# Optimization experiments

Measured on AMD Instinct MI355X. Metric: run time of the kernel, lower is better.

Reference implementation:

```python
import jax, jax.numpy as jnp
import numpy as np

B, S, D, H = 8, 1024, 1024, 16
DH = D // H


def setup_inputs() -> dict:
    key = jax.random.key(0)
    ks = jax.random.split(key, 7)
    scale = 1.0 / np.sqrt(DH)
    return {
        "sequences": jax.random.normal(ks[0], (B, S, D), dtype=jnp.float32),
        "Wq": jax.random.uniform(ks[1], (H, DH, DH), jnp.float32, -scale, scale),
        "bq": jax.random.uniform(ks[2], (H, DH), jnp.float32, -scale, scale),
        "Wk": jax.random.uniform(ks[3], (H, DH, DH), jnp.float32, -scale, scale),
        "bk": jax.random.uniform(ks[4], (H, DH), jnp.float32, -scale, scale),
        "Wv": jax.random.uniform(ks[5], (H, DH, DH), jnp.float32, -scale, scale),
        "bv": jax.random.uniform(ks[6], (H, DH), jnp.float32, -scale, scale),
    }


def reference(sequences, Wq, bq, Wk, bk, Wv, bv):
    # split channels into heads: [B,S,H,DH]
    x = sequences.reshape(B, S, H, DH)
    # per-head linear maps (torch Linear: y = x @ W.T + b)
    q = jnp.einsum("bshd,hed->bshe", x, Wq) + bq  # [B,S,H,DH]
    k = jnp.einsum("bshd,hed->bshe", x, Wk) + bk
    v = jnp.einsum("bshd,hed->bshe", x, Wv) + bv
    scores = jnp.einsum("bshd,bthd->bhst", q, k) / jnp.sqrt(jnp.asarray(DH, x.dtype))
    attn = jax.nn.softmax(scores, axis=-1)  # [B,H,S,S]
    out = jnp.einsum("bhst,bthd->bshd", attn, v)  # [B,S,H,DH]
    return out.reshape(B, S, D)
```

## Files before the change

### kernel.cpp

```cpp
#include <hip/hip_runtime.h>
#include <hip/hip_bf16.h>


constexpr int NB = 8, NS = 1024, ND = 1024, NH = 16, NDH = 64;

typedef __bf16 bf16x8 __attribute__((ext_vector_type(8)));
typedef float f32x4 __attribute__((ext_vector_type(4)));

__device__ __forceinline__ f32x4 mfma16(bf16x8 a, bf16x8 b, f32x4 c) {
  return __builtin_amdgcn_mfma_f32_16x16x32_bf16(a, b, c, 0, 0, 0);
}

__device__ __forceinline__ bf16x8 cvt2bf8(float4 lo, float4 hi) {
  bf16x8 r;
  r[0] = (__bf16)lo.x; r[1] = (__bf16)lo.y; r[2] = (__bf16)lo.z; r[3] = (__bf16)lo.w;
  r[4] = (__bf16)hi.x; r[5] = (__bf16)hi.y; r[6] = (__bf16)hi.z; r[7] = (__bf16)hi.w;
  return r;
}

__device__ __forceinline__ void gload16(const __hip_bfloat16* g, __hip_bfloat16* l) {
  __builtin_amdgcn_global_load_lds(
      (const __attribute__((address_space(1))) void*)g,
      (__attribute__((address_space(3))) void*)l, 16, 0, 0);
}

__global__ __launch_bounds__(256) void qkv_proj_kernel(
    const float* __restrict__ x,
    const float* __restrict__ Wq, const float* __restrict__ bq,
    const float* __restrict__ Wk, const float* __restrict__ bk,
    const float* __restrict__ Wv, const float* __restrict__ bv,
    __hip_bfloat16* __restrict__ Qo, __hip_bfloat16* __restrict__ Ko,
    __hip_bfloat16* __restrict__ Vt) {
  __shared__ __align__(16) __hip_bfloat16 Wlds[3][NDH][72];
  const int tid = threadIdx.x;
  const int wave = tid >> 6, lane = tid & 63;
  const int m = lane & 15, quad = lane >> 4;
  const int h = blockIdx.x & (NH - 1);
  const int sblk = blockIdx.x >> 4;

  const float* Ws[3] = {Wq + h * 4096, Wk + h * 4096, Wv + h * 4096};
#pragma unroll
  for (int mt = 0; mt < 3; mt++) {
#pragma unroll
    for (int p = 0; p < 4; p++) {
      int idx = (p * 256 + tid) * 4;
      float4 v = *(const float4*)(Ws[mt] + idx);
      __align__(8) __hip_bfloat16 t4[4] = {
          __float2bfloat16(v.x), __float2bfloat16(v.y),
          __float2bfloat16(v.z), __float2bfloat16(v.w)};
      *(uint2*)&Wlds[mt][idx >> 6][idx & 63] = *(const uint2*)t4;
    }
  }
  __syncthreads();

  float bq4[4][4], bk4[4][4], bvv[4];
#pragma unroll
  for (int nt = 0; nt < 4; nt++) {
    float4 a = *(const float4*)(bq + h * 64 + nt * 16 + quad * 4);
    float4 c = *(const float4*)(bk + h * 64 + nt * 16 + quad * 4);
    bq4[nt][0] = a.x; bq4[nt][1] = a.y; bq4[nt][2] = a.z; bq4[nt][3] = a.w;
    bk4[nt][0] = c.x; bk4[nt][1] = c.y; bk4[nt][2] = c.z; bk4[nt][3] = c.w;
    bvv[nt] = bv[h * 64 + nt * 16 + m];
  }

  const int rowbase = sblk * 256 + wave * 64;
  bf16x8 Xf[4][2];
#pragma unroll
  for (int st = 0; st < 4; st++) {
    const float* xp = x + (size_t)(rowbase + st * 16 + m) * ND + h * NDH + quad * 8;
#pragma unroll
    for (int c = 0; c < 2; c++) {
      float4 lo = *(const float4*)(xp + c * 32);
      float4 hi = *(const float4*)(xp + c * 32 + 4);
      Xf[st][c] = cvt2bf8(lo, hi);
    }
  }

  const int b = rowbase >> 10;
  const int s0 = rowbase & 1023;
  const float qscale = 0.18033688011112042f;

#pragma unroll
  for (int mt = 0; mt < 3; mt++) {
#pragma unroll
    for (int nt = 0; nt < 4; nt++) {
      bf16x8 w0 = *(const bf16x8*)&Wlds[mt][nt * 16 + m][quad * 8];
      bf16x8 w1 = *(const bf16x8*)&Wlds[mt][nt * 16 + m][32 + quad * 8];
#pragma unroll
      for (int st = 0; st < 4; st++) {
        f32x4 acc = {0.f, 0.f, 0.f, 0.f};
        if (mt < 2) {
          acc = mfma16(w0, Xf[st][0], acc);
          acc = mfma16(w1, Xf[st][1], acc);
          const int srow = s0 + st * 16 + m;
          __align__(8) __hip_bfloat16 t4[4];
          if (mt == 0) {
#pragma unroll
            for (int r = 0; r < 4; r++)
              t4[r] = __float2bfloat16((acc[r] + bq4[nt][r]) * qscale);
            *(uint2*)(Qo + ((size_t)(b * NH + h) * NS + srow) * NDH +
                      nt * 16 + quad * 4) = *(const uint2*)t4;
          } else {
#pragma unroll
            for (int r = 0; r < 4; r++)
              t4[r] = __float2bfloat16(acc[r] + bk4[nt][r]);
            *(uint2*)(Ko + ((size_t)(b * NH + h) * NS + srow) * NDH +
                      nt * 16 + quad * 4) = *(const uint2*)t4;
          }
        } else {
          acc = mfma16(Xf[st][0], w0, acc);
          acc = mfma16(Xf[st][1], w1, acc);
          __align__(8) __hip_bfloat16 t4[4];
#pragma unroll
          for (int r = 0; r < 4; r++) t4[r] = __float2bfloat16(acc[r] + bvv[nt]);
          *(uint2*)(Vt + ((size_t)(b * NH + h) * NDH + nt * 16 + m) * NS + s0 +
                    st * 16 + quad * 4) = *(const uint2*)t4;
        }
      }
    }
  }
}

__global__ __launch_bounds__(256, 3) void attn_kernel(
    const __hip_bfloat16* __restrict__ Q,
    const __hip_bfloat16* __restrict__ K,
    const __hip_bfloat16* __restrict__ Vt,
    float* __restrict__ out) {
  __shared__ __align__(16) __hip_bfloat16 Kt[2][64][64];
  __shared__ __align__(16) __hip_bfloat16 Vl[2][64][64];
  __shared__ __align__(16) __hip_bfloat16 Pt[4][2][16][64];

  const int tid = threadIdx.x;
  const int wave = tid >> 6, lane = tid & 63;
  const int m = lane & 15, quad = lane >> 4;

  const int xcd = blockIdx.x & 7;
  const int j = blockIdx.x >> 3;
  const int bh = xcd * 16 + (j & 15);
  const int qblk = j >> 4;
  const int qbase = qblk * 128 + wave * 32;

  const __hip_bfloat16* Qp = Q + (size_t)bh * NS * NDH;
  const __hip_bfloat16* Kp = K + (size_t)bh * NS * NDH;
  const __hip_bfloat16* Vp = Vt + (size_t)bh * NDH * NS;

  bf16x8 Bq[2][2];
#pragma unroll
  for (int g = 0; g < 2; g++)
#pragma unroll
    for (int c = 0; c < 2; c++)
      Bq[g][c] = *(const bf16x8*)(Qp + (size_t)(qbase + g * 16 + m) * NDH +
                                  c * 32 + quad * 8);

  f32x4 accO[2][4];
  f32x4 lsum[2];
#pragma unroll
  for (int g = 0; g < 2; g++) {
    lsum[g] = (f32x4){0.f, 0.f, 0.f, 0.f};
#pragma unroll
    for (int nt = 0; nt < 4; nt++) accO[g][nt] = (f32x4){0.f, 0.f, 0.f, 0.f};
  }
  bf16x8 ones;
#pragma unroll
  for (int i = 0; i < 8; i++) ones[i] = (__bf16)1.0f;

  const int r8 = lane >> 3;
  const int cs = (lane & 7) ^ r8;
  const int pc = quad ^ (m & 7);

#define STAGE(buf, tb)                                                        \
  {                                                                           \
    _Pragma("unroll") for (int p = 0; p < 2; p++) {                           \
      const int row = wave * 16 + p * 8;                                      \
      gload16(Kp + (size_t)((tb) * 64 + row + r8) * NDH + cs * 8,             \
              &Kt[buf][row][0]);                                              \
      gload16(Vp + (size_t)(row + r8) * NS + (tb) * 64 + cs * 8,              \
              &Vl[buf][row][0]);                                              \
    }                                                                         \
  }

  STAGE(0, 0);

  for (int tb = 0; tb < NS / 64; tb++) {
    const int cur = tb & 1;
    __syncthreads();
    if (tb + 1 < NS / 64) STAGE(cur ^ 1, tb + 1);

    f32x4 sc[2][4];
#pragma unroll
    for (int nt = 0; nt < 4; nt++) {
      bf16x8 k0 = *(const bf16x8*)&Kt[cur][nt * 16 + m][pc * 8];
      bf16x8 k1 = *(const bf16x8*)&Kt[cur][nt * 16 + m][(pc ^ 4) * 8];
#pragma unroll
      for (int g = 0; g < 2; g++) {
        f32x4 a = {0.f, 0.f, 0.f, 0.f};
        a = mfma16(k0, Bq[g][0], a);
        a = mfma16(k1, Bq[g][1], a);
        sc[g][nt] = a;
      }
    }
#pragma unroll
    for (int g = 0; g < 2; g++) {
#pragma unroll
      for (int nt = 0; nt < 4; nt++) {
        __align__(8) __hip_bfloat16 t4[4];
#pragma unroll
        for (int r = 0; r < 4; r++)
          t4[r] = __float2bfloat16(__builtin_exp2f(sc[g][nt][r]));
        const int c8 = (nt * 2 + (quad >> 1)) ^ (m & 7);
        *(uint2*)&Pt[wave][g][m][c8 * 8 + (quad & 1) * 4] = *(const uint2*)t4;
      }
    }
    __builtin_amdgcn_fence(__ATOMIC_SEQ_CST, "wavefront");
    bf16x8 Pf[2][2];
#pragma unroll
    for (int g = 0; g < 2; g++) {
      Pf[g][0] = *(const bf16x8*)&Pt[wave][g][m][pc * 8];
      Pf[g][1] = *(const bf16x8*)&Pt[wave][g][m][(pc ^ 4) * 8];
      lsum[g] = mfma16(Pf[g][0], ones, lsum[g]);
      lsum[g] = mfma16(Pf[g][1], ones, lsum[g]);
    }
#pragma unroll
    for (int nt = 0; nt < 4; nt++) {
      bf16x8 v0 = *(const bf16x8*)&Vl[cur][nt * 16 + m][pc * 8];
      bf16x8 v1 = *(const bf16x8*)&Vl[cur][nt * 16 + m][(pc ^ 4) * 8];
#pragma unroll
      for (int g = 0; g < 2; g++) {
        accO[g][nt] = mfma16(Pf[g][0], v0, accO[g][nt]);
        accO[g][nt] = mfma16(Pf[g][1], v1, accO[g][nt]);
      }
    }
  }
#undef STAGE

  const int b = bh >> 4, h = bh & (NH - 1);
#pragma unroll
  for (int g = 0; g < 2; g++) {
#pragma unroll
    for (int r = 0; r < 4; r++) {
      float inv = 1.0f / lsum[g][r];
      int srow = qbase + g * 16 + quad * 4 + r;
      float* op = out + (size_t)(b * NS + srow) * ND + h * NDH;
#pragma unroll
      for (int nt = 0; nt < 4; nt++) op[nt * 16 + m] = accO[g][nt][r] * inv;
    }
  }
}

extern "C" void kernel_launch(void* const* d_in, const int* in_sizes, int n_in,
                              void* d_out, int out_size, void* d_ws, size_t ws_size,
                              hipStream_t stream) {
  const float* x  = (const float*)d_in[0];
  const float* Wq = (const float*)d_in[1];
  const float* bq = (const float*)d_in[2];
  const float* Wk = (const float*)d_in[3];
  const float* bk = (const float*)d_in[4];
  const float* Wv = (const float*)d_in[5];
  const float* bv = (const float*)d_in[6];
  float* out = (float*)d_out;

  const size_t elems = (size_t)NB * NH * NS * NDH;
  __hip_bfloat16* Qw = (__hip_bfloat16*)d_ws;
  __hip_bfloat16* Kw = Qw + elems;
  __hip_bfloat16* Vw = Kw + elems;

  qkv_proj_kernel<<<512, 256, 0, stream>>>(x, Wq, bq, Wk, bk, Wv, bv, Qw, Kw, Vw);
  attn_kernel<<<1024, 256, 0, stream>>>(Qw, Kw, Vw, out);
}
```

Baseline: 162.5 us.

## Process query groups sequentially in attention to cut registers and raise occupancy

Restructures the attention inner loop so each 16-row query group computes scores, writes P and runs the PV MMA before the next group starts. This halves the live score registers and the P staging LDS buffer, which allows the launch-bounds occupancy hint to be raised from 3 to 4 blocks. It also replaces the bf16 conversion with a bit-trick round-and-pack using v_perm. In exchange, K and V fragments are reloaded from LDS once per group, the wavefront fence runs twice per tile, and the packed rounding differs slightly from round-to-nearest-even.

```diff
diff --git a/kernel.cpp b/kernel.cpp
--- a/kernel.cpp
+++ b/kernel.cpp
@@ -22,6 +22,12 @@
   __builtin_amdgcn_global_load_lds(
       (const __attribute__((address_space(1))) void*)g,
       (__attribute__((address_space(3))) void*)l, 16, 0, 0);
+}
+
+__device__ __forceinline__ unsigned pack_bf16(float hi, float lo) {
+  unsigned uh = __builtin_bit_cast(unsigned, hi) + 0x8000u;
+  unsigned ul = __builtin_bit_cast(unsigned, lo) + 0x8000u;
+  return __builtin_amdgcn_perm(uh, ul, 0x07060302u);
 }
 
 __global__ __launch_bounds__(256) void qkv_proj_kernel(
@@ -121,14 +127,14 @@
   }
 }
 
-__global__ __launch_bounds__(256, 3) void attn_kernel(
+__global__ __launch_bounds__(256, 4) void attn_kernel(
     const __hip_bfloat16* __restrict__ Q,
     const __hip_bfloat16* __restrict__ K,
     const __hip_bfloat16* __restrict__ Vt,
     float* __restrict__ out) {
   __shared__ __align__(16) __hip_bfloat16 Kt[2][64][64];
   __shared__ __align__(16) __hip_bfloat16 Vl[2][64][64];
-  __shared__ __align__(16) __hip_bfloat16 Pt[4][2][16][64];
+  __shared__ __align__(16) __hip_bfloat16 Pt[4][16][64];
 
   const int tid = threadIdx.x;
   const int wave = tid >> 6, lane = tid & 63;
@@ -186,48 +192,41 @@
     __syncthreads();
     if (tb + 1 < NS / 64) STAGE(cur ^ 1, tb + 1);
 
-    f32x4 sc[2][4];
-#pragma unroll
-    for (int nt = 0; nt < 4; nt++) {
-      bf16x8 k0 = *(const bf16x8*)&Kt[cur][nt * 16 + m][pc * 8];
-      bf16x8 k1 = *(const bf16x8*)&Kt[cur][nt * 16 + m][(pc ^ 4) * 8];
-#pragma unroll
-      for (int g = 0; g < 2; g++) {
+#pragma unroll
+    for (int g = 0; g < 2; g++) {
+      f32x4 sc[4];
+#pragma unroll
+      for (int nt = 0; nt < 4; nt++) {
+        bf16x8 k0 = *(const bf16x8*)&Kt[cur][nt * 16 + m][pc * 8];
+        bf16x8 k1 = *(const bf16x8*)&Kt[cur][nt * 16 + m][(pc ^ 4) * 8];
         f32x4 a = {0.f, 0.f, 0.f, 0.f};
         a = mfma16(k0, Bq[g][0], a);
         a = mfma16(k1, Bq[g][1], a);
-        sc[g][nt] = a;
-      }
-    }
-#pragma unroll
-    for (int g = 0; g < 2; g++) {
+        sc[nt] = a;
+      }
 #pragma unroll
       for (int nt = 0; nt < 4; nt++) {
-        __align__(8) __hip_bfloat16 t4[4];
-#pragma unroll
-        for (int r = 0; r < 4; r++)
-          t4[r] = __float2bfloat16(__builtin_exp2f(sc[g][nt][r]));
+        float e0 = __builtin_exp2f(sc[nt][0]);
+        float e1 = __builtin_exp2f(sc[nt][1]);
+        float e2 = __builtin_exp2f(sc[nt][2]);
+        float e3 = __builtin_exp2f(sc[nt][3]);
+        uint2 w;
+        w.x = pack_bf16(e1, e0);
+        w.y = pack_bf16(e3, e2);
         const int c8 = (nt * 2 + (quad >> 1)) ^ (m & 7);
-        *(uint2*)&Pt[wave][g][m][c8 * 8 + (quad & 1) * 4] = *(const uint2*)t4;
-      }
-    }
-    __builtin_amdgcn_fence(__ATOMIC_SEQ_CST, "wavefront");
-    bf16x8 Pf[2][2];
-#pragma unroll
-    for (int g = 0; g < 2; g++) {
-      Pf[g][0] = *(const bf16x8*)&Pt[wave][g][m][pc * 8];
-      Pf[g][1] = *(const bf16x8*)&Pt[wave][g][m][(pc ^ 4) * 8];
-      lsum[g] = mfma16(Pf[g][0], ones, lsum[g]);
-      lsum[g] = mfma16(Pf[g][1], ones, lsum[g]);
-    }
-#pragma unroll
-    for (int nt = 0; nt < 4; nt++) {
-      bf16x8 v0 = *(const bf16x8*)&Vl[cur][nt * 16 + m][pc * 8];
-      bf16x8 v1 = *(const bf16x8*)&Vl[cur][nt * 16 + m][(pc ^ 4) * 8];
-#pragma unroll
-      for (int g = 0; g < 2; g++) {
-        accO[g][nt] = mfma16(Pf[g][0], v0, accO[g][nt]);
-        accO[g][nt] = mfma16(Pf[g][1], v1, accO[g][nt]);
+        *(uint2*)&Pt[wave][m][c8 * 8 + (quad & 1) * 4] = w;
+      }
+      __builtin_amdgcn_fence(__ATOMIC_SEQ_CST, "wavefront");
+      bf16x8 P0 = *(const bf16x8*)&Pt[wave][m][pc * 8];
+      bf16x8 P1 = *(const bf16x8*)&Pt[wave][m][(pc ^ 4) * 8];
+      lsum[g] = mfma16(P0, ones, lsum[g]);
+      lsum[g] = mfma16(P1, ones, lsum[g]);
+#pragma unroll
+      for (int nt = 0; nt < 4; nt++) {
+        bf16x8 v0 = *(const bf16x8*)&Vl[cur][nt * 16 + m][pc * 8];
+        bf16x8 v1 = *(const bf16x8*)&Vl[cur][nt * 16 + m][(pc ^ 4) * 8];
+        accO[g][nt] = mfma16(P0, v0, accO[g][nt]);
+        accO[g][nt] = mfma16(P1, v1, accO[g][nt]);
       }
     }
   }
```

New measurement: 161.1 us. About the same (-0.9%).
